# Kernel optimization log

Hardware: AMD Instinct MI355X
Metric: run time of the kernel (lower is better)

The kernel has to match this reference:

```python
import jax, jax.numpy as jnp
import numpy as np

D_MODEL = 1024
N_HEADS = 16
EPS_LN = 1e-5


def _ln(x, g, b):
    m = jnp.mean(x, axis=-1, keepdims=True)
    v = jnp.mean((x - m) ** 2, axis=-1, keepdims=True)
    return (x - m) * jax.lax.rsqrt(v + EPS_LN) * g + b


def setup_inputs() -> dict:
    key = jax.random.key(0)
    ks = jax.random.split(key, 8)
    B, S, D = 8, 8192, D_MODEL
    # xavier_uniform with gain 1/sqrt(2) for square (D,D) weights
    limit = (1.0 / np.sqrt(2.0)) * np.sqrt(6.0 / (D + D))
    def w(k):
        return jax.random.uniform(k, (D, D), jnp.float32, -limit, limit)
    return {
        "x": jax.random.normal(ks[0], (B, S, D), jnp.float32),
        "query": jax.random.normal(ks[1], (1, 1, D), jnp.float32) * 0.02,
        "norm_g": jnp.ones((D,), jnp.float32), "norm_b": jnp.zeros((D,), jnp.float32),
        "nq_g": jnp.ones((D,), jnp.float32), "nq_b": jnp.zeros((D,), jnp.float32),
        "nk_g": jnp.ones((D,), jnp.float32), "nk_b": jnp.zeros((D,), jnp.float32),
        "nv_g": jnp.ones((D,), jnp.float32), "nv_b": jnp.zeros((D,), jnp.float32),
        "no_g": jnp.ones((D,), jnp.float32), "no_b": jnp.zeros((D,), jnp.float32),
        "Wq": w(ks[2]), "bq": jnp.zeros((D,), jnp.float32),
        "Wk": w(ks[3]), "bk": jnp.zeros((D,), jnp.float32),
        "Wv": w(ks[4]), "bv": jnp.zeros((D,), jnp.float32),
        "Wo": w(ks[5]), "bo": jnp.zeros((D,), jnp.float32),
    }


def reference(x, query, norm_g, norm_b, nq_g, nq_b, nk_g, nk_b, nv_g, nv_b,
              no_g, no_b, Wq, bq, Wk, bk, Wv, bv, Wo, bo):
    B, S, D = x.shape
    H = N_HEADS
    dk = D // H
    # PoolingLayer.forward (dropout in eval mode -> identity)
    xn = _ln(x, norm_g, norm_b)                      # [B,S,D]
    q_in = jnp.broadcast_to(query, (B, 1, D))        # [B,1,D]
    # AttentionLayer: per-input LayerNorms then projections
    qn = _ln(q_in, nq_g, nq_b)
    kn = _ln(xn, nk_g, nk_b)
    vn = _ln(xn, nv_g, nv_b)
    q = (qn @ Wq.T + bq).reshape(B, 1, H, dk)        # [B,1,H,dk]
    k = (kn @ Wk.T + bk).reshape(B, S, H, dk)        # [B,S,H,dk]
    v = (vn @ Wv.T + bv).reshape(B, S, H, dk)        # [B,S,H,dk]
    # FullAttention, q_len == 1 (decode-style)
    scale = 1.0 / jnp.sqrt(jnp.float32(dk))
    scores = jnp.einsum("bqhd,bshd->bhqs", q * scale, k)  # [B,H,1,S]
    smax = jnp.max(scores, axis=-1, keepdims=True)
    sexp = jnp.exp(scores - smax)
    attn = sexp / (jnp.sum(sexp, axis=-1, keepdims=True) + 1e-9)
    attn = jnp.clip(attn, 1e-9, 1.0)
    out = jnp.einsum("bhqs,bshd->bqhd", attn, v).reshape(B, 1, D)
    out = out @ Wo.T + bo
    out = _ln(out, no_g, no_b)
    return out[:, 0, :]                               # [B,D]
```

## Files before the change

kernel.cpp:

```cpp
#include <hip/hip_runtime.h>
#include <math.h>

#define D 1024
#define S 8192
#define B 8
#define H 16
#define NROWS (B * S)
#define EPS_LN 1e-5f

typedef _Float16 h2 __attribute__((ext_vector_type(2)));
typedef __fp16 half8 __attribute__((ext_vector_type(8)));
typedef float f32x4 __attribute__((ext_vector_type(4)));

__device__ __forceinline__ float wred_sum(float v) {
#pragma unroll
  for (int m = 1; m < 64; m <<= 1) v += __shfl_xor(v, m, 64);
  return v;
}
__device__ __forceinline__ h2 pkh(float a, float b) {
#if __has_builtin(__builtin_amdgcn_cvt_pkrtz)
  return __builtin_bit_cast(h2, __builtin_amdgcn_cvt_pkrtz(a, b));
#else
  h2 r; r.x = (_Float16)a; r.y = (_Float16)b; return r;
#endif
}
__device__ __forceinline__ float fdot2(h2 a, h2 b, float c) {
#if __has_builtin(__builtin_amdgcn_fdot2)
  typedef __fp16 fp16v2 __attribute__((ext_vector_type(2)));
  return __builtin_amdgcn_fdot2(__builtin_bit_cast(fp16v2, a),
                                __builtin_bit_cast(fp16v2, b), c, false);
#else
  return c + (float)a.x * (float)b.x + (float)a.y * (float)b.y;
#endif
}
__device__ __forceinline__ h2 bch(unsigned int u) { return __builtin_bit_cast(h2, u); }
__device__ __forceinline__ unsigned int hbits(h2 v) {
  return __builtin_bit_cast(unsigned int, v);
}

__global__ void k_ln256(const float* __restrict__ in, const float* __restrict__ g,
                        const float* __restrict__ bb, float* __restrict__ out) {
  const int b = blockIdx.x, t = threadIdx.x;
  float4 v = ((const float4*)(in + (size_t)b * D))[t];
  float s = v.x + v.y + v.z + v.w;
  float s2 = fmaf(v.x, v.x, fmaf(v.y, v.y, fmaf(v.z, v.z, v.w * v.w)));
  __shared__ float red[8];
  float ws = wred_sum(s), ws2 = wred_sum(s2);
  const int lane = t & 63, wv = t >> 6;
  if (!lane) { red[wv] = ws; red[wv + 4] = ws2; }
  __syncthreads();
  ws = red[0] + red[1] + red[2] + red[3];
  ws2 = red[4] + red[5] + red[6] + red[7];
  const float m = ws * (1.f / D);
  const float rs = rsqrtf(ws2 * (1.f / D) - m * m + EPS_LN);
  const float4 gg = ((const float4*)g)[t], bv = ((const float4*)bb)[t];
  float4 o;
  o.x = (v.x - m) * rs * gg.x + bv.x;
  o.y = (v.y - m) * rs * gg.y + bv.y;
  o.z = (v.z - m) * rs * gg.z + bv.z;
  o.w = (v.w - m) * rs * gg.w + bv.w;
  ((float4*)(out + (size_t)b * D))[t] = o;
}

__global__ void k_qln(const float* __restrict__ query, const float* __restrict__ ng,
                      const float* __restrict__ nb, const float* __restrict__ Wq,
                      const float* __restrict__ bq, float* __restrict__ qv) {
  __shared__ float qn[D];
  __shared__ float red[8];
  const int t = threadIdx.x, lane = t & 63, wv = t >> 6;
  float4 v = ((const float4*)query)[t];
  float s = v.x + v.y + v.z + v.w;
  float s2 = fmaf(v.x, v.x, fmaf(v.y, v.y, fmaf(v.z, v.z, v.w * v.w)));
  float ws = wred_sum(s), ws2 = wred_sum(s2);
  if (!lane) { red[wv] = ws; red[wv + 4] = ws2; }
  __syncthreads();
  ws = red[0] + red[1] + red[2] + red[3];
  ws2 = red[4] + red[5] + red[6] + red[7];
  const float m = ws * (1.f / D);
  const float rs = rsqrtf(ws2 * (1.f / D) - m * m + EPS_LN);
  const float4 gg = ((const float4*)ng)[t], bv = ((const float4*)nb)[t];
  float4 o;
  o.x = (v.x - m) * rs * gg.x + bv.x;
  o.y = (v.y - m) * rs * gg.y + bv.y;
  o.z = (v.z - m) * rs * gg.z + bv.z;
  o.w = (v.w - m) * rs * gg.w + bv.w;
  ((float4*)qn)[t] = o;
  __syncthreads();
  const int j = blockIdx.x * 4 + wv;
  const float4* wr = (const float4*)(Wq + (size_t)j * D);
  float acc = 0.f;
#pragma unroll
  for (int k = 0; k < 4; k++) {
    float4 a = ((const float4*)qn)[lane + 64 * k], w = wr[lane + 64 * k];
    acc = fmaf(a.x, w.x, acc); acc = fmaf(a.y, w.y, acc);
    acc = fmaf(a.z, w.z, acc); acc = fmaf(a.w, w.w, acc);
  }
  acc = wred_sum(acc);
  if (!lane) qv[j] = acc + bq[j];
}

__global__ void k_prep0G(const float* __restrict__ g, const float* __restrict__ b,
                         float* __restrict__ sconst, uint4* __restrict__ gt,
                         uint4* __restrict__ g2t, uint4* __restrict__ gbt,
                         float* __restrict__ hc, float* __restrict__ Cbuf) {
  const int t = threadIdx.x;
  float4 gv = ((const float4*)g)[t], bv = ((const float4*)b)[t];
  float sg = gv.x + gv.y + gv.z + gv.w;
  float sb = bv.x + bv.y + bv.z + bv.w;
  float sbb = bv.x * bv.x + bv.y * bv.y + bv.z * bv.z + bv.w * bv.w;
  float sgb = gv.x * bv.x + gv.y * bv.y + gv.z * bv.z + gv.w * bv.w;
  float sgg = gv.x * gv.x + gv.y * gv.y + gv.z * gv.z + gv.w * gv.w;
  __shared__ float red[4][5];
  sg = wred_sum(sg); sb = wred_sum(sb); sbb = wred_sum(sbb);
  sgb = wred_sum(sgb); sgg = wred_sum(sgg);
  const int lane = t & 63, wv = t >> 6;
  if (!lane) { red[wv][0] = sg; red[wv][1] = sb; red[wv][2] = sbb; red[wv][3] = sgb; red[wv][4] = sgg; }
  __syncthreads();
  if (t < 5) sconst[t] = red[0][t] + red[1][t] + red[2][t] + red[3][t];
  if (t < 16) ((float4*)hc)[t] = make_float4(0.f, 0.f, 0.f, 0.f);
  if (t < 128) ((float4*)Cbuf)[t] = make_float4(0.f, 0.f, 0.f, 0.f);
  if (t < 128) {
    const int grp = t;
    const int k0 = (grp >> 2) * 32 + (grp & 3) * 8;
    unsigned int a[4], bb2[4], c[4];
#pragma unroll
    for (int p = 0; p < 4; p++) {
      const int k = k0 + 2 * p;
      const float g0 = g[k], g1v = g[k + 1];
      const float b0 = b[k], b1v = b[k + 1];
      a[p] = hbits(pkh(g0, g1v));
      bb2[p] = hbits(pkh(g0 * g0, g1v * g1v));
      c[p] = hbits(pkh(g0 * b0, g1v * b1v));
    }
    gt[grp] = make_uint4(a[0], a[1], a[2], a[3]);
    g2t[grp] = make_uint4(bb2[0], bb2[1], bb2[2], bb2[3]);
    gbt[grp] = make_uint4(c[0], c[1], c[2], c[3]);
  }
}

__global__ void k_uprep64(const float* __restrict__ qv, const float* __restrict__ Wk,
                          const float* __restrict__ g1, const float* __restrict__ b1,
                          const float* __restrict__ kgw, const float* __restrict__ kbw,
                          float* __restrict__ hc, uint4* __restrict__ B1) {
  __shared__ float sUf[256];
  __shared__ float qh[64];
  __shared__ float red[4][4];
  const int h = blockIdx.x >> 2, q = blockIdx.x & 3, t = threadIdx.x;
  if (t < 64) qh[t] = qv[h * 64 + t];
  __syncthreads();
  const int d = q * 256 + t;
  float acc = 0.f;
#pragma unroll 4
  for (int e = 0; e < 64; e++)
    acc = fmaf(qh[e], Wk[(size_t)(h * 64 + e) * D + d], acc);
  acc *= 0.125f;
  sUf[t] = acc;
  const float gv = g1[d], bv = b1[d], kgv = kgw[d], kbv = kbw[d];
  float p2 = acc * kgv * bv;
  float p3 = acc * gv * kgv;
  float p4 = acc * kgv;
  float p5 = acc * kbv;
  p2 = wred_sum(p2); p3 = wred_sum(p3); p4 = wred_sum(p4); p5 = wred_sum(p5);
  const int lane = t & 63, wv = t >> 6;
  if (!lane) { red[wv][0] = p2; red[wv][1] = p3; red[wv][2] = p4; red[wv][3] = p5; }
  __syncthreads();
  if (t < 4)
    atomicAdd(&hc[t * 16 + h], red[0][t] + red[1][t] + red[2][t] + red[3][t]);
  if (t < 32) {
    const int grp = q * 32 + t;
    const int k0 = (grp >> 2) * 32 + (grp & 3) * 8;
    const int kl = k0 - q * 256;
    unsigned int wv2[4];
#pragma unroll
    for (int p = 0; p < 4; p++) {
      const int k = kl + 2 * p, kg2 = k0 + 2 * p;
      const float e0 = sUf[k] * g1[kg2] * kgw[kg2];
      const float e1 = sUf[k + 1] * g1[kg2 + 1] * kgw[kg2 + 1];
      wv2[p] = hbits(pkh(e0, e1));
    }
    B1[grp * 16 + h] = make_uint4(wv2[0], wv2[1], wv2[2], wv2[3]);
  }
}

__global__ __launch_bounds__(256) void k_fused(
    const float* __restrict__ x, const uint4* __restrict__ B1,
    const uint4* __restrict__ gt, const uint4* __restrict__ g2t,
    const uint4* __restrict__ gbt, const float* __restrict__ hc,
    const float* __restrict__ sconst, float* __restrict__ part,
    float* __restrict__ Cbuf, int niter, int bpb) {
  __shared__ __align__(16) uint4 sB[2048];
  __shared__ __align__(16) uint4 sg[128], sg2[128], sgb[128];
  __shared__ __align__(16) unsigned int xl[4][16 * 133];
  __shared__ __align__(16) f32x4 sred[4][64];
  __shared__ float stat[4][16][6];
  for (int i = threadIdx.x; i < 2048; i += 256) sB[i] = B1[i];
  if (threadIdx.x < 128) {
    sg[threadIdx.x] = gt[threadIdx.x];
    sg2[threadIdx.x] = g2t[threadIdx.x];
    sgb[threadIdx.x] = gbt[threadIdx.x];
  }
  __syncthreads();
  const int lane = threadIdx.x & 63, w = threadIdx.x >> 6;
  const int col = lane & 15, kg = lane >> 4;
  const float c2 = hc[col], c3 = hc[16 + col], c4 = hc[32 + col], c5 = hc[48 + col];
  const float Sg1 = sconst[0], Sb1 = sconst[1], Sbbc = sconst[2];
  const float Sgbc = sconst[3], Sggc = sconst[4];
  const h2 one = {(_Float16)1.f, (_Float16)1.f};
  const int sh = (col & 1) * 16;
  f32x4 accpv[16];
#pragma unroll
  for (int c = 0; c < 16; c++) accpv[c] = (f32x4){0.f, 0.f, 0.f, 0.f};
  float dh0 = 0.f, dh1 = 0.f, dh2 = 0.f, dh3 = 0.f;
  const int rbase = blockIdx.x * (16 * niter);
#pragma unroll 1
  for (int it = 0; it < niter; it++) {
    const int r0 = rbase + it * 16;
    const float* xrow = x + (size_t)(r0 + col) * D + w * 256 + kg * 8;
    f32x4 sacc = {0.f, 0.f, 0.f, 0.f};
    float S0 = 0, S1 = 0, Sa = 0, Sb = 0, Sc = 0, Sd = 0;
#pragma unroll
    for (int ks = 0; ks < 8; ks++) {
      const float4 A0 = *(const float4*)(xrow + ks * 32);
      const float4 A1 = *(const float4*)(xrow + ks * 32 + 4);
      const h2 a0 = pkh(A0.x, A0.y), a1 = pkh(A0.z, A0.w);
      const h2 a2 = pkh(A1.x, A1.y), a3 = pkh(A1.z, A1.w);
      const int gidx = (w * 8 + ks) * 4 + kg;
      const uint4 bu = sB[gidx * 16 + col];
      const uint4 gu = sg[gidx], g2u = sg2[gidx], gbu = sgb[gidx];
      S0 = fdot2(a0, one, S0); S0 = fdot2(a1, one, S0);
      S0 = fdot2(a2, one, S0); S0 = fdot2(a3, one, S0);
      S1 = fdot2(a0, a0, S1); S1 = fdot2(a1, a1, S1);
      S1 = fdot2(a2, a2, S1); S1 = fdot2(a3, a3, S1);
      const h2 g0 = bch(gu.x), g1p = bch(gu.y), g2p = bch(gu.z), g3p = bch(gu.w);
      Sa = fdot2(g0, a0, Sa); Sa = fdot2(g1p, a1, Sa);
      Sa = fdot2(g2p, a2, Sa); Sa = fdot2(g3p, a3, Sa);
      const h2 G0 = bch(g2u.x), G1 = bch(g2u.y), G2 = bch(g2u.z), G3 = bch(g2u.w);
      Sb = fdot2(G0, a0, Sb); Sb = fdot2(G1, a1, Sb);
      Sb = fdot2(G2, a2, Sb); Sb = fdot2(G3, a3, Sb);
      Sc = fdot2(G0, a0 * a0, Sc); Sc = fdot2(G1, a1 * a1, Sc);
      Sc = fdot2(G2, a2 * a2, Sc); Sc = fdot2(G3, a3 * a3, Sc);
      const h2 Q0 = bch(gbu.x), Q1 = bch(gbu.y), Q2 = bch(gbu.z), Q3 = bch(gbu.w);
      Sd = fdot2(Q0, a0, Sd); Sd = fdot2(Q1, a1, Sd);
      Sd = fdot2(Q2, a2, Sd); Sd = fdot2(Q3, a3, Sd);
      union { h2 p[4]; half8 v; } ua;
      ua.p[0] = a0; ua.p[1] = a1; ua.p[2] = a2; ua.p[3] = a3;
      sacc = __builtin_amdgcn_mfma_f32_16x16x32_f16(
          ua.v, __builtin_bit_cast(half8, bu), sacc, 0, 0, 0);
      uint4 xw;
      xw.x = hbits(a0); xw.y = hbits(a1); xw.z = hbits(a2); xw.w = hbits(a3);
      *(uint4*)&xl[w][col * 133 + kg * 4 + ks * 16] = xw;
    }
#pragma unroll
    for (int m = 16; m < 64; m <<= 1) {
      S0 += __shfl_xor(S0, m, 64); S1 += __shfl_xor(S1, m, 64);
      Sa += __shfl_xor(Sa, m, 64); Sb += __shfl_xor(Sb, m, 64);
      Sc += __shfl_xor(Sc, m, 64); Sd += __shfl_xor(Sd, m, 64);
    }
    if (lane < 16) {
      stat[w][lane][0] = S0; stat[w][lane][1] = S1; stat[w][lane][2] = Sa;
      stat[w][lane][3] = Sb; stat[w][lane][4] = Sc; stat[w][lane][5] = Sd;
    }
    sred[w][lane] = sacc;
    __syncthreads();
    f32x4 full = sred[0][lane];
    full += sred[1][lane]; full += sred[2][lane]; full += sred[3][lane];
    float T0 = 0, T1v = 0, Ta = 0, Tb = 0, Tc = 0, Td = 0;
#pragma unroll
    for (int ww = 0; ww < 4; ww++) {
      T0 += stat[ww][col][0]; T1v += stat[ww][col][1]; Ta += stat[ww][col][2];
      Tb += stat[ww][col][3]; Tc += stat[ww][col][4]; Td += stat[ww][col][5];
    }
    const float m1 = T0 * (1.f / D);
    const float rs1 = rsqrtf(T1v * (1.f / D) - m1 * m1 + EPS_LN);
    const float m2 = (rs1 * (Ta - m1 * Sg1) + Sb1) * (1.f / D);
    const float sxn2 = rs1 * rs1 * Tc + 2.f * rs1 * (Td - m1 * rs1 * Tb) +
                       (Sbbc - 2.f * m1 * rs1 * Sgbc + m1 * m1 * rs1 * rs1 * Sggc);
    const float rs2 = rsqrtf(sxn2 * (1.f / D) - m2 * m2 + EPS_LN);
    const float v1 = rs1 * rs2, v2 = v1 * m1, v3 = rs2, v4 = rs2 * m2;
    float ap_[4];
#pragma unroll
    for (int j = 0; j < 4; j++) {
      const int rj = kg * 4 + j;
      const float w1 = __shfl(v1, rj, 64), w2 = __shfl(v2, rj, 64);
      const float w3 = __shfl(v3, rj, 64), w4 = __shfl(v4, rj, 64);
      const float s = w1 * full[j] - w2 * c3 + w3 * c2 - w4 * c4 + c5;
      const float e = __expf(s);
      ap_[j] = e * w1;
      if (w == 0) { dh0 += e; dh1 += e * w3; dh2 += e * w2; dh3 += e * w4; }
    }
    union { h2 p[4]; half8 v; } ap;
    ap.p[0] = pkh(ap_[0], ap_[1]); ap.p[1] = pkh(ap_[2], ap_[3]);
    ap.p[2] = bch(0u); ap.p[3] = bch(0u);
    const unsigned int* xw = xl[w];
#pragma unroll
    for (int c = 0; c < 16; c++) {
      const int bidx = c * 8 + (col >> 1);
      const unsigned int r0w = xw[(kg * 4 + 0) * 133 + bidx];
      const unsigned int r1w = xw[(kg * 4 + 1) * 133 + bidx];
      const unsigned int r2w = xw[(kg * 4 + 2) * 133 + bidx];
      const unsigned int r3w = xw[(kg * 4 + 3) * 133 + bidx];
      union { unsigned int u[4]; half8 v; } bb;
      bb.u[0] = ((r0w >> sh) & 0xffffu) | (((r1w >> sh) & 0xffffu) << 16);
      bb.u[1] = ((r2w >> sh) & 0xffffu) | (((r3w >> sh) & 0xffffu) << 16);
      bb.u[2] = 0u; bb.u[3] = 0u;
      accpv[c] = __builtin_amdgcn_mfma_f32_16x16x32_f16(ap.v, bb.v, accpv[c], 0, 0, 0);
    }
    __syncthreads();
  }
  if (w == 0) {
#pragma unroll
    for (int m = 16; m < 64; m <<= 1) {
      dh0 += __shfl_xor(dh0, m, 64); dh1 += __shfl_xor(dh1, m, 64);
      dh2 += __shfl_xor(dh2, m, 64); dh3 += __shfl_xor(dh3, m, 64);
    }
    if (lane < 16) {
      const int b = blockIdx.x / bpb;
      float* cb = Cbuf + (b * 16 + lane) * 4;
      atomicAdd(cb + 0, dh0); atomicAdd(cb + 1, dh1);
      atomicAdd(cb + 2, dh2); atomicAdd(cb + 3, dh3);
    }
  }
  float* po = part + ((size_t)blockIdx.x * 16) * 1024 + w * 256;
#pragma unroll
  for (int c = 0; c < 16; c++) {
#pragma unroll
    for (int reg = 0; reg < 4; reg++) {
      const int h = kg * 4 + reg;
      po[(size_t)h * 1024 + c * 16 + col] = accpv[c][reg];
    }
  }
}

__global__ void k_reduce(const float* __restrict__ part, const float* __restrict__ Cbuf,
                         const float* __restrict__ g1, const float* __restrict__ b1,
                         const float* __restrict__ vg, const float* __restrict__ vb,
                         float* __restrict__ vpool, int bpb) {
  const int b = blockIdx.x >> 4, h = blockIdx.x & 15;
  const int t = threadIdx.x, d = t * 4;
  float4 a = make_float4(0.f, 0.f, 0.f, 0.f);
  for (int k = 0; k < bpb; k++) {
    const float4 p =
        *(const float4*)(part + ((size_t)((b * bpb + k) * 16 + h)) * 1024 + d);
    a.x += p.x; a.y += p.y; a.z += p.z; a.w += p.w;
  }
  const float4 C = ((const float4*)Cbuf)[b * 16 + h];
  const float inv = 1.f / C.x;
  const float C1n = C.y * inv, C2n = C.z * inv, C3n = C.w * inv;
  const float4 gv = ((const float4*)g1)[t], bv = ((const float4*)b1)[t];
  const float4 vgv = ((const float4*)vg)[t], vbv = ((const float4*)vb)[t];
  float4 o;
  o.x = vgv.x * (gv.x * (a.x * inv - C2n) + bv.x * C1n - C3n) + vbv.x;
  o.y = vgv.y * (gv.y * (a.y * inv - C2n) + bv.y * C1n - C3n) + vbv.y;
  o.z = vgv.z * (gv.z * (a.z * inv - C2n) + bv.z * C1n - C3n) + vbv.z;
  o.w = vgv.w * (gv.w * (a.w * inv - C2n) + bv.w * C1n - C3n) + vbv.w;
  *(float4*)(vpool + ((size_t)b * H + h) * D + d) = o;
}

__global__ void k_proj8(const float* __restrict__ src, const float* __restrict__ W,
                        const float* __restrict__ bias, float* __restrict__ out,
                        int bstride, int hstride) {
  const int j = blockIdx.x, lane = threadIdx.x;
  const int h = j >> 6;
  const float4* wr = (const float4*)(W + (size_t)j * D);
  float acc[8];
#pragma unroll
  for (int b = 0; b < 8; b++) acc[b] = 0.f;
#pragma unroll
  for (int k = 0; k < 4; k++) {
    const float4 w4 = wr[lane + 64 * k];
#pragma unroll
    for (int b = 0; b < 8; b++) {
      const float4 s4 =
          ((const float4*)(src + (size_t)b * bstride + (size_t)h * hstride))[lane + 64 * k];
      acc[b] = fmaf(w4.x, s4.x, acc[b]); acc[b] = fmaf(w4.y, s4.y, acc[b]);
      acc[b] = fmaf(w4.z, s4.z, acc[b]); acc[b] = fmaf(w4.w, s4.w, acc[b]);
    }
  }
#pragma unroll
  for (int b = 0; b < 8; b++) acc[b] = wred_sum(acc[b]);
  if (!lane) {
    const float bj = bias[j];
#pragma unroll
    for (int b = 0; b < 8; b++) out[(size_t)b * D + j] = acc[b] + bj;
  }
}

extern "C" void kernel_launch(void* const* d_in, const int* in_sizes, int n_in,
                              void* d_out, int out_size, void* d_ws, size_t ws_size,
                              hipStream_t stream) {
  const float* x = (const float*)d_in[0];
  const float* query = (const float*)d_in[1];
  const float* norm_g = (const float*)d_in[2];
  const float* norm_b = (const float*)d_in[3];
  const float* nq_g = (const float*)d_in[4];
  const float* nq_b = (const float*)d_in[5];
  const float* nk_g = (const float*)d_in[6];
  const float* nk_b = (const float*)d_in[7];
  const float* nv_g = (const float*)d_in[8];
  const float* nv_b = (const float*)d_in[9];
  const float* no_g = (const float*)d_in[10];
  const float* no_b = (const float*)d_in[11];
  const float* Wq = (const float*)d_in[12];
  const float* bq = (const float*)d_in[13];
  const float* Wk = (const float*)d_in[14];
  const float* Wv = (const float*)d_in[16];
  const float* bv = (const float*)d_in[17];
  const float* Wo = (const float*)d_in[18];
  const float* bo = (const float*)d_in[19];

  char* ws = (char*)d_ws;
  float* qv = (float*)(ws + 0);
  uint4* B1 = (uint4*)(ws + 4096);
  uint4* gt = (uint4*)(ws + 36864);
  uint4* g2t = (uint4*)(ws + 38912);
  uint4* gbt = (uint4*)(ws + 40960);
  float* hc = (float*)(ws + 43008);
  float* sconst = (float*)(ws + 43264);
  float* Cbuf = (float*)(ws + 43328);
  float* vpool = (float*)(ws + 45568);
  float* av = (float*)(ws + 569856);
  float* yb = (float*)(ws + 602624);
  float* part = (float*)(ws + 635904);

  int NBLK = 512;
  if (635904ull + (size_t)NBLK * 16 * 1024 * 4 > ws_size) NBLK = 256;
  const int niter = NROWS / (16 * NBLK);
  const int bpb = NBLK / B;

  k_qln<<<256, 256, 0, stream>>>(query, nq_g, nq_b, Wq, bq, qv);
  k_prep0G<<<1, 256, 0, stream>>>(norm_g, norm_b, sconst, gt, g2t, gbt, hc, Cbuf);
  k_uprep64<<<64, 256, 0, stream>>>(qv, Wk, norm_g, norm_b, nk_g, nk_b, hc, B1);
  k_fused<<<NBLK, 256, 0, stream>>>(x, B1, gt, g2t, gbt, hc, sconst, part, Cbuf,
                                    niter, bpb);
  k_reduce<<<128, 256, 0, stream>>>(part, Cbuf, norm_g, norm_b, nv_g, nv_b, vpool, bpb);
  k_proj8<<<1024, 64, 0, stream>>>(vpool, Wv, bv, av, H * D, D);
  k_proj8<<<1024, 64, 0, stream>>>(av, Wo, bo, yb, D, 0);
  k_ln256<<<8, 256, 0, stream>>>(yb, no_g, no_b, (float*)d_out);
}
```

Before: 114.3 us.

## Reload x tile from cache for PV MFMA instead of LDS staging; double-buffer reductions

The fp16 copy of the x tile is no longer staged in LDS for the attention-weighted V accumulation. Each lane instead re-reads the same 16-row tile from global memory (expected to hit L2 or L1) with a column mapping that avoids the shift-and-mask repacking. The reduction buffers are double-buffered by iteration parity, which removes the second barrier per iteration, and launch bounds request 3 blocks per SM. The partial outputs are now written as float4. In exchange, x traffic through the cache doubles and the reloads are converted to fp16 a second time.

```diff
diff --git a/kernel.cpp b/kernel.cpp
--- a/kernel.cpp
+++ b/kernel.cpp
@@ -182,7 +182,7 @@
   }
 }
 
-__global__ __launch_bounds__(256) void k_fused(
+__global__ __launch_bounds__(256, 3) void k_fused(
     const float* __restrict__ x, const uint4* __restrict__ B1,
     const uint4* __restrict__ gt, const uint4* __restrict__ g2t,
     const uint4* __restrict__ gbt, const float* __restrict__ hc,
@@ -190,9 +190,8 @@
     float* __restrict__ Cbuf, int niter, int bpb) {
   __shared__ __align__(16) uint4 sB[2048];
   __shared__ __align__(16) uint4 sg[128], sg2[128], sgb[128];
-  __shared__ __align__(16) unsigned int xl[4][16 * 133];
-  __shared__ __align__(16) f32x4 sred[4][64];
-  __shared__ float stat[4][16][6];
+  __shared__ __align__(16) f32x4 sred[2][4][64];
+  __shared__ float stat[2][4][16][6];
   for (int i = threadIdx.x; i < 2048; i += 256) sB[i] = B1[i];
   if (threadIdx.x < 128) {
     sg[threadIdx.x] = gt[threadIdx.x];
@@ -206,7 +205,6 @@
   const float Sg1 = sconst[0], Sb1 = sconst[1], Sbbc = sconst[2];
   const float Sgbc = sconst[3], Sggc = sconst[4];
   const h2 one = {(_Float16)1.f, (_Float16)1.f};
-  const int sh = (col & 1) * 16;
   f32x4 accpv[16];
 #pragma unroll
   for (int c = 0; c < 16; c++) accpv[c] = (f32x4){0.f, 0.f, 0.f, 0.f};
@@ -214,6 +212,7 @@
   const int rbase = blockIdx.x * (16 * niter);
 #pragma unroll 1
   for (int it = 0; it < niter; it++) {
+    const int p = it & 1;
     const int r0 = rbase + it * 16;
     const float* xrow = x + (size_t)(r0 + col) * D + w * 256 + kg * 8;
     f32x4 sacc = {0.f, 0.f, 0.f, 0.f};
@@ -242,13 +241,10 @@
       const h2 Q0 = bch(gbu.x), Q1 = bch(gbu.y), Q2 = bch(gbu.z), Q3 = bch(gbu.w);
       Sd = fdot2(Q0, a0, Sd); Sd = fdot2(Q1, a1, Sd);
       Sd = fdot2(Q2, a2, Sd); Sd = fdot2(Q3, a3, Sd);
-      union { h2 p[4]; half8 v; } ua;
-      ua.p[0] = a0; ua.p[1] = a1; ua.p[2] = a2; ua.p[3] = a3;
+      union { h2 pp[4]; half8 v; } ua;
+      ua.pp[0] = a0; ua.pp[1] = a1; ua.pp[2] = a2; ua.pp[3] = a3;
       sacc = __builtin_amdgcn_mfma_f32_16x16x32_f16(
           ua.v, __builtin_bit_cast(half8, bu), sacc, 0, 0, 0);
-      uint4 xw;
-      xw.x = hbits(a0); xw.y = hbits(a1); xw.z = hbits(a2); xw.w = hbits(a3);
-      *(uint4*)&xl[w][col * 133 + kg * 4 + ks * 16] = xw;
     }
 #pragma unroll
     for (int m = 16; m < 64; m <<= 1) {
@@ -257,18 +253,18 @@
       Sc += __shfl_xor(Sc, m, 64); Sd += __shfl_xor(Sd, m, 64);
     }
     if (lane < 16) {
-      stat[w][lane][0] = S0; stat[w][lane][1] = S1; stat[w][lane][2] = Sa;
-      stat[w][lane][3] = Sb; stat[w][lane][4] = Sc; stat[w][lane][5] = Sd;
-    }
-    sred[w][lane] = sacc;
+      stat[p][w][lane][0] = S0; stat[p][w][lane][1] = S1; stat[p][w][lane][2] = Sa;
+      stat[p][w][lane][3] = Sb; stat[p][w][lane][4] = Sc; stat[p][w][lane][5] = Sd;
+    }
+    sred[p][w][lane] = sacc;
     __syncthreads();
-    f32x4 full = sred[0][lane];
-    full += sred[1][lane]; full += sred[2][lane]; full += sred[3][lane];
+    f32x4 full = sred[p][0][lane];
+    full += sred[p][1][lane]; full += sred[p][2][lane]; full += sred[p][3][lane];
     float T0 = 0, T1v = 0, Ta = 0, Tb = 0, Tc = 0, Td = 0;
 #pragma unroll
     for (int ww = 0; ww < 4; ww++) {
-      T0 += stat[ww][col][0]; T1v += stat[ww][col][1]; Ta += stat[ww][col][2];
-      Tb += stat[ww][col][3]; Tc += stat[ww][col][4]; Td += stat[ww][col][5];
+      T0 += stat[p][ww][col][0]; T1v += stat[p][ww][col][1]; Ta += stat[p][ww][col][2];
+      Tb += stat[p][ww][col][3]; Tc += stat[p][ww][col][4]; Td += stat[p][ww][col][5];
     }
     const float m1 = T0 * (1.f / D);
     const float rs1 = rsqrtf(T1v * (1.f / D) - m1 * m1 + EPS_LN);
@@ -288,24 +284,31 @@
       ap_[j] = e * w1;
       if (w == 0) { dh0 += e; dh1 += e * w3; dh2 += e * w2; dh3 += e * w4; }
     }
-    union { h2 p[4]; half8 v; } ap;
-    ap.p[0] = pkh(ap_[0], ap_[1]); ap.p[1] = pkh(ap_[2], ap_[3]);
-    ap.p[2] = bch(0u); ap.p[3] = bch(0u);
-    const unsigned int* xw = xl[w];
-#pragma unroll
-    for (int c = 0; c < 16; c++) {
-      const int bidx = c * 8 + (col >> 1);
-      const unsigned int r0w = xw[(kg * 4 + 0) * 133 + bidx];
-      const unsigned int r1w = xw[(kg * 4 + 1) * 133 + bidx];
-      const unsigned int r2w = xw[(kg * 4 + 2) * 133 + bidx];
-      const unsigned int r3w = xw[(kg * 4 + 3) * 133 + bidx];
-      union { unsigned int u[4]; half8 v; } bb;
-      bb.u[0] = ((r0w >> sh) & 0xffffu) | (((r1w >> sh) & 0xffffu) << 16);
-      bb.u[1] = ((r2w >> sh) & 0xffffu) | (((r3w >> sh) & 0xffffu) << 16);
-      bb.u[2] = 0u; bb.u[3] = 0u;
-      accpv[c] = __builtin_amdgcn_mfma_f32_16x16x32_f16(ap.v, bb.v, accpv[c], 0, 0, 0);
-    }
-    __syncthreads();
+    union { h2 pp[4]; half8 v; } ap;
+    ap.pp[0] = pkh(ap_[0], ap_[1]); ap.pp[1] = pkh(ap_[2], ap_[3]);
+    ap.pp[2] = bch(0u); ap.pp[3] = bch(0u);
+    const float* xpv = x + (size_t)(r0 + kg * 4) * D + w * 256 + col * 16;
+#pragma unroll
+    for (int cg = 0; cg < 4; cg++) {
+      const float4 xA = *(const float4*)(xpv + cg * 4);
+      const float4 xB = *(const float4*)(xpv + D + cg * 4);
+      const float4 xC = *(const float4*)(xpv + 2 * D + cg * 4);
+      const float4 xD = *(const float4*)(xpv + 3 * D + cg * 4);
+      const float fA[4] = {xA.x, xA.y, xA.z, xA.w};
+      const float fB[4] = {xB.x, xB.y, xB.z, xB.w};
+      const float fC[4] = {xC.x, xC.y, xC.z, xC.w};
+      const float fD[4] = {xD.x, xD.y, xD.z, xD.w};
+#pragma unroll
+      for (int e2 = 0; e2 < 4; e2++) {
+        const int c = cg * 4 + e2;
+        union { unsigned int u[4]; half8 v; } bb;
+        bb.u[0] = hbits(pkh(fA[e2], fB[e2]));
+        bb.u[1] = hbits(pkh(fC[e2], fD[e2]));
+        bb.u[2] = 0u; bb.u[3] = 0u;
+        accpv[c] =
+            __builtin_amdgcn_mfma_f32_16x16x32_f16(ap.v, bb.v, accpv[c], 0, 0, 0);
+      }
+    }
   }
   if (w == 0) {
 #pragma unroll
@@ -320,13 +323,16 @@
       atomicAdd(cb + 2, dh2); atomicAdd(cb + 3, dh3);
     }
   }
-  float* po = part + ((size_t)blockIdx.x * 16) * 1024 + w * 256;
-#pragma unroll
-  for (int c = 0; c < 16; c++) {
-#pragma unroll
-    for (int reg = 0; reg < 4; reg++) {
-      const int h = kg * 4 + reg;
-      po[(size_t)h * 1024 + c * 16 + col] = accpv[c][reg];
+  float* po = part + ((size_t)blockIdx.x * 16) * 1024 + w * 256 + col * 16;
+#pragma unroll
+  for (int reg = 0; reg < 4; reg++) {
+    const int h = kg * 4 + reg;
+#pragma unroll
+    for (int cg = 0; cg < 4; cg++) {
+      float4 v;
+      v.x = accpv[cg * 4 + 0][reg]; v.y = accpv[cg * 4 + 1][reg];
+      v.z = accpv[cg * 4 + 2][reg]; v.w = accpv[cg * 4 + 3][reg];
+      *(float4*)(po + (size_t)h * 1024 + cg * 4) = v;
     }
   }
 }
```

After: 162.7 us. 1.42x slower.
